# Performance work log

Hardware: AMD Instinct MI355X
Metric: run time of the kernel (lower is better)

Reference implementation:

```python
import jax, jax.numpy as jnp
import numpy as np

B, L, R, K = 4, 512, 512, 16
DN, DE = 128, 64
HOPI, CNNC = 32, 32


def _conv2d(x, w, b, pad):
    # x: (B,C,H,W), w: (O,I,kh,kw)
    y = jax.lax.conv_general_dilated(x, w, (1, 1), [(pad, pad), (pad, pad)],
                                     dimension_numbers=('NCHW', 'OIHW', 'NCHW'))
    return y + b[None, :, None, None]


def setup_inputs() -> dict:
    key = jax.random.key(0)
    ks = jax.random.split(key, 16)
    s = lambda d: 1.0 / np.sqrt(d)
    inp = {
        'ligand_node_features': jax.random.normal(ks[0], (B, L, DN), jnp.float32),
        'ligand_edge_features': jax.random.normal(ks[1], (B, L, K, DE), jnp.float32),
        'receptor_node_features': jax.random.normal(ks[2], (B, R, DN), jnp.float32),
        'receptor_edge_features': jax.random.normal(ks[3], (B, R, K, DE), jnp.float32),
        # GNN params
        'WN': jax.random.uniform(ks[4], (DN, DN), jnp.float32, -s(DN), s(DN)),
        'bN': jax.random.uniform(ks[5], (DN,), jnp.float32, -s(DN), s(DN)),
        'WE': jax.random.uniform(ks[6], (DN, DE), jnp.float32, -s(DE), s(DE)),
        'bE': jax.random.uniform(ks[7], (DN,), jnp.float32, -s(DE), s(DE)),
        # HOPI linear: (out, 2*DN)
        'Wp': jax.random.uniform(ks[8], (HOPI, 2 * DN), jnp.float32, -s(2 * DN), s(2 * DN)),
        'bp': jax.random.uniform(ks[9], (HOPI,), jnp.float32, -s(2 * DN), s(2 * DN)),
        # CNN params
        'Wc1': jax.random.uniform(ks[10], (CNNC, HOPI, 3, 3), jnp.float32, -s(HOPI * 9), s(HOPI * 9)),
        'bc1': jax.random.uniform(ks[11], (CNNC,), jnp.float32, -s(HOPI * 9), s(HOPI * 9)),
        'Wc2': jax.random.uniform(ks[12], (CNNC, CNNC, 3, 3), jnp.float32, -s(CNNC * 9), s(CNNC * 9)),
        'bc2': jax.random.uniform(ks[13], (CNNC,), jnp.float32, -s(CNNC * 9), s(CNNC * 9)),
        'Wc3': jax.random.uniform(ks[14], (1, CNNC, 1, 1), jnp.float32, -s(CNNC), s(CNNC)),
        'bc3': jax.random.uniform(ks[15], (1,), jnp.float32, -s(CNNC), s(CNNC)),
    }
    return inp


def _gnn(node, edge, WN, bN, WE, bE):
    # node: (B,N,DN), edge: (B,N,K,DE) -> (B,N,DN)
    hn = jnp.einsum('bnd,od->bno', node, WN) + bN          # (B,N,DN)
    he = jnp.einsum('bnke,oe->bnko', edge, WE) + bE        # (B,N,K,DN)
    Z = jnp.tanh(hn[:, :, None, :] + he)                   # (B,N,K,DN)
    return node + Z.mean(axis=2)


def reference(ligand_node_features, ligand_edge_features, receptor_node_features,
              receptor_edge_features, WN, bN, WE, bE, Wp, bp,
              Wc1, bc1, Wc2, bc2, Wc3, bc3):
    lig = _gnn(ligand_node_features, ligand_edge_features, WN, bN, WE, bE)      # (B,L,DN)
    rec = _gnn(receptor_node_features, receptor_edge_features, WN, bN, WE, bE)  # (B,R,DN)
    # HOPI: linear(cat(lig_i, rec_j)) = lig@Wl^T + rec@Wr^T + b, broadcast over pairs
    Wl, Wr = Wp[:, :DN], Wp[:, DN:]
    pl = jnp.einsum('bld,od->blo', lig, Wl)                 # (B,L,HOPI)
    pr = jnp.einsum('brd,od->bro', rec, Wr)                 # (B,R,HOPI)
    P = pl[:, :, None, :] + pr[:, None, :, :] + bp          # (B,L,R,HOPI)
    x = jnp.transpose(P, (0, 3, 1, 2))                      # (B,HOPI,L,R)
    x = jax.nn.relu(_conv2d(x, Wc1, bc1, 1))
    x = jax.nn.relu(_conv2d(x, Wc2, bc2, 1))
    x = _conv2d(x, Wc3, bc3, 0)                             # (B,1,L,R)
    return jax.nn.sigmoid(x)[:, 0]                          # (B,L,R)
```

## Files before the change

### kernel.cpp

```cpp
#include <hip/hip_runtime.h>
#include <hip/hip_bf16.h>
#include <math.h>


typedef __attribute__((ext_vector_type(8))) short short8v;
typedef __attribute__((ext_vector_type(4))) float f32x4;

__device__ __forceinline__ unsigned pack_bf16_2(float x, float y) {
    __hip_bfloat16 hx = __float2bfloat16(x);
    __hip_bfloat16 hy = __float2bfloat16(y);
    unsigned short ux = *(unsigned short*)&hx;
    unsigned short uy = *(unsigned short*)&hy;
    return (unsigned)ux | ((unsigned)uy << 16);
}

__global__ __launch_bounds__(256) void prep_weights(
    const float* __restrict__ Wc1, const float* __restrict__ Wc2,
    const float* __restrict__ WN, const float* __restrict__ WE,
    const float* __restrict__ Wp,
    float* __restrict__ WA, float* __restrict__ WB,
    unsigned short* __restrict__ W2F,
    float* __restrict__ WN4, float* __restrict__ WE4,
    float* __restrict__ WpT4)
{
    const int t = blockIdx.x * 256 + threadIdx.x;

    if (t < 9216) {
        const int f    = t >> 9;
        const int lane = (t >> 3) & 63;
        const int j    = t & 7;
        const int tap  = f >> 1;
        const int h    = f & 1;
        const int co   = h * 16 + (lane & 15);
        const int ci   = (lane >> 4) * 8 + j;
        const float w  = Wc2[(co * 32 + ci) * 9 + tap];
        __hip_bfloat16 hb = __float2bfloat16(w);
        W2F[t] = *(unsigned short*)&hb;

        const int tap1 = t >> 10;
        const int ci1  = (t >> 5) & 31;
        const int co1  = t & 31;
        if (tap1 < 3) {
            const int k = tap1;
            const float* w1 = Wc1 + (co1 * 32 + ci1) * 9;
            float w0 = w1[k * 3 + 0], wq = w1[k * 3 + 1], w2 = w1[k * 3 + 2];
            WA[((0 * 3 + k) * 32 + ci1) * 32 + co1] = wq + w2;
            WA[((1 * 3 + k) * 32 + ci1) * 32 + co1] = w0 + wq + w2;
            WA[((2 * 3 + k) * 32 + ci1) * 32 + co1] = w0 + wq;
            float q0 = w1[0 * 3 + k], q1 = w1[1 * 3 + k], q2 = w1[2 * 3 + k];
            WB[((0 * 3 + k) * 32 + ci1) * 32 + co1] = q1 + q2;
            WB[((1 * 3 + k) * 32 + ci1) * 32 + co1] = q0 + q1 + q2;
            WB[((2 * 3 + k) * 32 + ci1) * 32 + co1] = q0 + q1;
        }
    }
    if (t < 16384) {
        const int d4 = t >> 9, o = (t >> 2) & 127, j = t & 3;
        WN4[t] = WN[o * 128 + d4 * 4 + j];
    }
    if (t < 8192) {
        const int e4 = t >> 9, o = (t >> 2) & 127, j = t & 3;
        WE4[t] = WE[o * 64 + e4 * 4 + j];
    }
    if (t < 8192) {
        const int d4 = t >> 8, c = (t >> 2) & 63, j = t & 3;
        const int s = c >> 5, po = c & 31;
        WpT4[t] = Wp[po * 256 + s * 128 + d4 * 4 + j];
    }
}

__global__ __launch_bounds__(128, 4) void gnn_proj_kernel(
    const float* __restrict__ lig_node, const float* __restrict__ lig_edge,
    const float* __restrict__ rec_node, const float* __restrict__ rec_edge,
    const float* __restrict__ WN4, const float* __restrict__ bN,
    const float* __restrict__ WE4, const float* __restrict__ bE,
    const float* __restrict__ WpT4, const float* __restrict__ bp,
    float* __restrict__ pl, float* __restrict__ prb)
{
    const int blk  = blockIdx.x;
    const int side = blk >> 11;
    const int b    = (blk >> 9) & 3;
    const int n    = blk & 511;
    const float* node = (side ? rec_node : lig_node) + (b * 512 + n) * 128;
    const float* edge = (side ? rec_edge : lig_edge) + (b * 512 + n) * 1024;

    __shared__ float s_node[128];
    __shared__ float s_edge[1024];
    __shared__ float s_out[128];

    const int tid = threadIdx.x;
    s_node[tid] = node[tid];
    ((float4*)s_edge)[tid]       = ((const float4*)edge)[tid];
    ((float4*)s_edge)[tid + 128] = ((const float4*)edge)[tid + 128];
    __syncthreads();

    const int o = tid;

    float4 h4 = make_float4(0.f, 0.f, 0.f, 0.f);
    const float4* wn4 = (const float4*)WN4 + o;
    const float4* sn4 = (const float4*)s_node;
    #pragma unroll 1
    for (int d4 = 0; d4 < 32; ++d4) {
        const float4 w = wn4[d4 * 128];
        const float4 x = sn4[d4];
        h4.x = fmaf(w.x, x.x, h4.x);
        h4.y = fmaf(w.y, x.y, h4.y);
        h4.z = fmaf(w.z, x.z, h4.z);
        h4.w = fmaf(w.w, x.w, h4.w);
    }
    const float base = (h4.x + h4.y) + (h4.z + h4.w) + bN[o] + bE[o];

    float acc[16];
    #pragma unroll
    for (int k = 0; k < 16; ++k) acc[k] = 0.f;
    const float4* we4 = (const float4*)WE4 + o;
    const float4* se4 = (const float4*)s_edge;
    #pragma unroll 1
    for (int e4 = 0; e4 < 16; ++e4) {
        const float4 w = we4[e4 * 128];
        #pragma unroll
        for (int k = 0; k < 16; ++k) {
            const float4 s = se4[k * 16 + e4];
            acc[k] = fmaf(w.x, s.x, fmaf(w.y, s.y,
                     fmaf(w.z, s.z, fmaf(w.w, s.w, acc[k]))));
        }
    }

    float ssum = 0.f;
    #pragma unroll
    for (int k = 0; k < 16; ++k) {
        const float ex = __expf(2.f * (base + acc[k]));
        ssum += 1.f - 2.f * __builtin_amdgcn_rcpf(ex + 1.f);
    }
    s_out[o] = s_node[o] + ssum * 0.0625f;
    __syncthreads();

    if (tid < 32) {
        const int c = side * 32 + tid;
        const float4* wp4 = (const float4*)WpT4 + c;
        const float4* so4 = (const float4*)s_out;
        float4 a4 = make_float4(0.f, 0.f, 0.f, 0.f);
        #pragma unroll 1
        for (int d4 = 0; d4 < 32; ++d4) {
            const float4 w = wp4[d4 * 64];
            const float4 x = so4[d4];
            a4.x = fmaf(w.x, x.x, a4.x);
            a4.y = fmaf(w.y, x.y, a4.y);
            a4.z = fmaf(w.z, x.z, a4.z);
            a4.w = fmaf(w.w, x.w, a4.w);
        }
        const float vv = (a4.x + a4.y) + (a4.z + a4.w) + (side ? bp[tid] : 0.f);
        (side ? prb : pl)[(b * 512 + n) * 32 + tid] = vv;
    }
}

__global__ __launch_bounds__(256) void uv_kernel(
    const float* __restrict__ pl, const float* __restrict__ prb,
    const float* __restrict__ WA, const float* __restrict__ WB,
    const float* __restrict__ bc1,
    float* __restrict__ u, float* __restrict__ v)
{
    const int idx = blockIdx.x * 256 + threadIdx.x;
    const int uv = idx >> 16;
    const int b  = (idx >> 14) & 3;
    const int l  = (idx >> 5) & 511;
    const int co = idx & 31;

    const float* p = (uv ? prb : pl) + (b * 512) * 32;
    const float* W = (uv ? WB : WA);
    float acc0 = uv ? 0.f : bc1[co];
    float acc1 = acc0, acc2 = acc0;
    #pragma unroll
    for (int d = 0; d < 3; ++d) {
        const int ln = l + d - 1;
        if (ln < 0 || ln >= 512) continue;
        const float* pv = p + ln * 32;
        const float* w0 = W + ((0 * 3 + d) * 32) * 32 + co;
        const float* w1 = W + ((1 * 3 + d) * 32) * 32 + co;
        const float* w2 = W + ((2 * 3 + d) * 32) * 32 + co;
        #pragma unroll
        for (int ci = 0; ci < 32; ++ci) {
            const float x = pv[ci];
            acc0 = fmaf(w0[ci * 32], x, acc0);
            acc1 = fmaf(w1[ci * 32], x, acc1);
            acc2 = fmaf(w2[ci * 32], x, acc2);
        }
    }
    float* dst = uv ? v : u;
    const int base = (b * 512 + l) * 32 + co;
    dst[0 * 65536 + base] = acc0;
    dst[1 * 65536 + base] = acc1;
    dst[2 * 65536 + base] = acc2;
}

__global__ __launch_bounds__(256) void conv_fused_kernel(
    const float* __restrict__ u, const float* __restrict__ v,
    const unsigned short* __restrict__ W2F,
    const float* __restrict__ bc2,
    const float* __restrict__ Wc3, const float* __restrict__ bc3,
    float* __restrict__ out)
{
    const int tc = blockIdx.x, tr = blockIdx.y, b = blockIdx.z;
    const int l0 = tr * 16, r0 = tc * 16;
    __shared__ unsigned short sY1[324 * 40];
    __shared__ float sU[18 * 36];
    __shared__ float sV[18 * 36];
    const int tid = threadIdx.x;

    for (int t = tid; t < 288; t += 256) {
        const int which = (t >= 144);
        const int s = which ? t - 144 : t;
        const int row = s >> 3, c4 = s & 7;
        const int pos = (which ? r0 : l0) - 1 + row;
        float4 val = make_float4(0.f, 0.f, 0.f, 0.f);
        if (pos >= 0 && pos < 512) {
            const float* src = (which ? v : u) + ((1 * 4 + b) * 512 + pos) * 32;
            val = ((const float4*)src)[c4];
        }
        ((float4*)((which ? sV : sU) + row * 36))[c4] = val;
    }
    __syncthreads();

    for (int p = tid; p < 324; p += 256) {
        const int i = p / 18, j = p - i * 18;
        const int l = l0 + i - 1, r = r0 + j - 1;
        uint4 q0 = make_uint4(0u, 0u, 0u, 0u), q1 = q0, q2 = q0, q3 = q0;
        if ((l >= 0) & (l < 512) & (r >= 0) & (r < 512)) {
            float y[32];
            const bool edge = (r == 0) | (r == 511) | (l == 0) | (l == 511);
            if (!edge) {
                const float4* up = (const float4*)&sU[i * 36];
                const float4* vp = (const float4*)&sV[j * 36];
                #pragma unroll
                for (int c4 = 0; c4 < 8; ++c4) {
                    const float4 a = up[c4], q = vp[c4];
                    y[c4 * 4 + 0] = fmaxf(a.x + q.x, 0.f);
                    y[c4 * 4 + 1] = fmaxf(a.y + q.y, 0.f);
                    y[c4 * 4 + 2] = fmaxf(a.z + q.z, 0.f);
                    y[c4 * 4 + 3] = fmaxf(a.w + q.w, 0.f);
                }
            } else {
                const int cr = (r == 0) ? 0 : (r == 511) ? 2 : 1;
                const int cl = (l == 0) ? 0 : (l == 511) ? 2 : 1;
                const float4* up = (const float4*)&u[((cr * 4 + b) * 512 + l) * 32];
                const float4* vp = (const float4*)&v[((cl * 4 + b) * 512 + r) * 32];
                #pragma unroll
                for (int c4 = 0; c4 < 8; ++c4) {
                    const float4 a = up[c4], q = vp[c4];
                    y[c4 * 4 + 0] = fmaxf(a.x + q.x, 0.f);
                    y[c4 * 4 + 1] = fmaxf(a.y + q.y, 0.f);
                    y[c4 * 4 + 2] = fmaxf(a.z + q.z, 0.f);
                    y[c4 * 4 + 3] = fmaxf(a.w + q.w, 0.f);
                }
            }
            q0 = make_uint4(pack_bf16_2(y[0], y[1]),  pack_bf16_2(y[2], y[3]),
                            pack_bf16_2(y[4], y[5]),  pack_bf16_2(y[6], y[7]));
            q1 = make_uint4(pack_bf16_2(y[8], y[9]),  pack_bf16_2(y[10], y[11]),
                            pack_bf16_2(y[12], y[13]), pack_bf16_2(y[14], y[15]));
            q2 = make_uint4(pack_bf16_2(y[16], y[17]), pack_bf16_2(y[18], y[19]),
                            pack_bf16_2(y[20], y[21]), pack_bf16_2(y[22], y[23]));
            q3 = make_uint4(pack_bf16_2(y[24], y[25]), pack_bf16_2(y[26], y[27]),
                            pack_bf16_2(y[28], y[29]), pack_bf16_2(y[30], y[31]));
        }
        uint4* dst = (uint4*)&sY1[p * 40];
        dst[0] = q0; dst[1] = q1; dst[2] = q2; dst[3] = q3;
    }

    const int lane = tid & 63;
    const int wv   = tid >> 6;
    const int m    = lane & 15;
    const int kc   = lane >> 4;
    short8v bf[18];
    #pragma unroll
    for (int f = 0; f < 18; ++f)
        bf[f] = *(const short8v*)&W2F[(f * 64 + lane) * 8];
    const float bc2_0 = bc2[m],      bc2_1 = bc2[m + 16];
    const float wc3_0 = Wc3[m],      wc3_1 = Wc3[m + 16];
    const float bc3v  = bc3[0];

    __syncthreads();

    #pragma unroll 1
    for (int i = 0; i < 4; ++i) {
        const int ty = wv * 4 + i;
        f32x4 acc0 = {0.f, 0.f, 0.f, 0.f};
        f32x4 acc1 = {0.f, 0.f, 0.f, 0.f};
        #pragma unroll
        for (int dy = 0; dy < 3; ++dy) {
            #pragma unroll
            for (int dx = 0; dx < 3; ++dx) {
                const short8v a = *(const short8v*)
                    &sY1[((ty + dy) * 18 + m + dx) * 40 + kc * 8];
                const int t = dy * 3 + dx;
                acc0 = __builtin_amdgcn_mfma_f32_16x16x32_bf16(a, bf[t * 2 + 0], acc0, 0, 0, 0);
                acc1 = __builtin_amdgcn_mfma_f32_16x16x32_bf16(a, bf[t * 2 + 1], acc1, 0, 0, 0);
            }
        }
        #pragma unroll
        for (int reg = 0; reg < 4; ++reg) {
            float vlt = fmaxf(acc0[reg] + bc2_0, 0.f) * wc3_0
                      + fmaxf(acc1[reg] + bc2_1, 0.f) * wc3_1;
            #pragma unroll
            for (int s = 1; s < 16; s <<= 1)
                vlt += __shfl_xor(vlt, s, 64);
            if (m == reg) {
                const int tx = kc * 4 + reg;
                const float sig = 1.f / (1.f + expf(-(vlt + bc3v)));
                out[(b * 512 + l0 + ty) * 512 + (r0 + tx)] = sig;
            }
        }
    }
}

extern "C" void kernel_launch(void* const* d_in, const int* in_sizes, int n_in,
                              void* d_out, int out_size, void* d_ws, size_t ws_size,
                              hipStream_t stream) {
    const float* lig_node = (const float*)d_in[0];
    const float* lig_edge = (const float*)d_in[1];
    const float* rec_node = (const float*)d_in[2];
    const float* rec_edge = (const float*)d_in[3];
    const float* WN  = (const float*)d_in[4];
    const float* bN  = (const float*)d_in[5];
    const float* WE  = (const float*)d_in[6];
    const float* bE  = (const float*)d_in[7];
    const float* Wp  = (const float*)d_in[8];
    const float* bp  = (const float*)d_in[9];
    const float* Wc1 = (const float*)d_in[10];
    const float* bc1 = (const float*)d_in[11];
    const float* Wc2 = (const float*)d_in[12];
    const float* bc2 = (const float*)d_in[13];
    const float* Wc3 = (const float*)d_in[14];
    const float* bc3 = (const float*)d_in[15];
    float* out = (float*)d_out;

    float* ws  = (float*)d_ws;
    float* pl   = ws;
    float* prb  = ws + 65536;
    float* WA   = ws + 131072;
    float* WB   = ws + 140288;
    unsigned short* W2F = (unsigned short*)(ws + 149504);
    float* u    = ws + 158720;
    float* v    = ws + 355328;
    float* WN4  = ws + 551936;
    float* WE4  = ws + 568320;
    float* WpT4 = ws + 576512;

    hipLaunchKernelGGL(prep_weights, dim3(64), dim3(256), 0, stream,
                       Wc1, Wc2, WN, WE, Wp, WA, WB, W2F, WN4, WE4, WpT4);
    hipLaunchKernelGGL(gnn_proj_kernel, dim3(4096), dim3(128), 0, stream,
                       lig_node, lig_edge, rec_node, rec_edge,
                       WN4, bN, WE4, bE, WpT4, bp, pl, prb);
    hipLaunchKernelGGL(uv_kernel, dim3(512), dim3(256), 0, stream,
                       pl, prb, WA, WB, bc1, u, v);
    hipLaunchKernelGGL(conv_fused_kernel, dim3(32, 32, 4), dim3(256), 0, stream,
                       u, v, W2F, bc2, Wc3, bc3, out);
}
```

Baseline: 187.4 us.

## Process four column tiles per conv block with double-buffered V prefetch

Each conv block now handles four consecutive 16-column tiles instead of one. The sU row data and the B-fragment weight registers are loaded once and reused across all four tiles, while the next tile's V halo rows are prefetched into a second shared buffer during the current tile's build. Blocks that do not touch the image border skip the per-pixel boundary checks. The aim is to amortize per-block setup and weight loads, at the cost of a 4x smaller grid (1024 blocks) and an extra barrier per tile.

```diff
diff --git a/kernel.cpp b/kernel.cpp
--- a/kernel.cpp
+++ b/kernel.cpp
@@ -199,70 +199,25 @@
     const float* __restrict__ Wc3, const float* __restrict__ bc3,
     float* __restrict__ out)
 {
-    const int tc = blockIdx.x, tr = blockIdx.y, b = blockIdx.z;
-    const int l0 = tr * 16, r0 = tc * 16;
+    const int x = blockIdx.x, tr = blockIdx.y, b = blockIdx.z;
+    const int l0 = tr * 16;
     __shared__ unsigned short sY1[324 * 40];
     __shared__ float sU[18 * 36];
-    __shared__ float sV[18 * 36];
+    __shared__ float sV[2][18 * 36];
     const int tid = threadIdx.x;
+    const bool edge_block = (x == 0) | (x == 7) | (tr == 0) | (tr == 31);
 
     for (int t = tid; t < 288; t += 256) {
         const int which = (t >= 144);
         const int s = which ? t - 144 : t;
         const int row = s >> 3, c4 = s & 7;
-        const int pos = (which ? r0 : l0) - 1 + row;
+        const int pos = (which ? x * 64 : l0) - 1 + row;
         float4 val = make_float4(0.f, 0.f, 0.f, 0.f);
         if (pos >= 0 && pos < 512) {
             const float* src = (which ? v : u) + ((1 * 4 + b) * 512 + pos) * 32;
             val = ((const float4*)src)[c4];
         }
-        ((float4*)((which ? sV : sU) + row * 36))[c4] = val;
-    }
-    __syncthreads();
-
-    for (int p = tid; p < 324; p += 256) {
-        const int i = p / 18, j = p - i * 18;
-        const int l = l0 + i - 1, r = r0 + j - 1;
-        uint4 q0 = make_uint4(0u, 0u, 0u, 0u), q1 = q0, q2 = q0, q3 = q0;
-        if ((l >= 0) & (l < 512) & (r >= 0) & (r < 512)) {
-            float y[32];
-            const bool edge = (r == 0) | (r == 511) | (l == 0) | (l == 511);
-            if (!edge) {
-                const float4* up = (const float4*)&sU[i * 36];
-                const float4* vp = (const float4*)&sV[j * 36];
-                #pragma unroll
-                for (int c4 = 0; c4 < 8; ++c4) {
-                    const float4 a = up[c4], q = vp[c4];
-                    y[c4 * 4 + 0] = fmaxf(a.x + q.x, 0.f);
-                    y[c4 * 4 + 1] = fmaxf(a.y + q.y, 0.f);
-                    y[c4 * 4 + 2] = fmaxf(a.z + q.z, 0.f);
-                    y[c4 * 4 + 3] = fmaxf(a.w + q.w, 0.f);
-                }
-            } else {
-                const int cr = (r == 0) ? 0 : (r == 511) ? 2 : 1;
-                const int cl = (l == 0) ? 0 : (l == 511) ? 2 : 1;
-                const float4* up = (const float4*)&u[((cr * 4 + b) * 512 + l) * 32];
-                const float4* vp = (const float4*)&v[((cl * 4 + b) * 512 + r) * 32];
-                #pragma unroll
-                for (int c4 = 0; c4 < 8; ++c4) {
-                    const float4 a = up[c4], q = vp[c4];
-                    y[c4 * 4 + 0] = fmaxf(a.x + q.x, 0.f);
-                    y[c4 * 4 + 1] = fmaxf(a.y + q.y, 0.f);
-                    y[c4 * 4 + 2] = fmaxf(a.z + q.z, 0.f);
-                    y[c4 * 4 + 3] = fmaxf(a.w + q.w, 0.f);
-                }
-            }
-            q0 = make_uint4(pack_bf16_2(y[0], y[1]),  pack_bf16_2(y[2], y[3]),
-                            pack_bf16_2(y[4], y[5]),  pack_bf16_2(y[6], y[7]));
-            q1 = make_uint4(pack_bf16_2(y[8], y[9]),  pack_bf16_2(y[10], y[11]),
-                            pack_bf16_2(y[12], y[13]), pack_bf16_2(y[14], y[15]));
-            q2 = make_uint4(pack_bf16_2(y[16], y[17]), pack_bf16_2(y[18], y[19]),
-                            pack_bf16_2(y[20], y[21]), pack_bf16_2(y[22], y[23]));
-            q3 = make_uint4(pack_bf16_2(y[24], y[25]), pack_bf16_2(y[26], y[27]),
-                            pack_bf16_2(y[28], y[29]), pack_bf16_2(y[30], y[31]));
-        }
-        uint4* dst = (uint4*)&sY1[p * 40];
-        dst[0] = q0; dst[1] = q1; dst[2] = q2; dst[3] = q3;
+        ((float4*)((which ? sV[0] : sU) + row * 36))[c4] = val;
     }
 
     const int lane = tid & 63;
@@ -280,34 +235,127 @@
     __syncthreads();
 
     #pragma unroll 1
-    for (int i = 0; i < 4; ++i) {
-        const int ty = wv * 4 + i;
-        f32x4 acc0 = {0.f, 0.f, 0.f, 0.f};
-        f32x4 acc1 = {0.f, 0.f, 0.f, 0.f};
-        #pragma unroll
-        for (int dy = 0; dy < 3; ++dy) {
+    for (int tt = 0; tt < 4; ++tt) {
+        const int r0 = (x * 4 + tt) * 16;
+        const float* sVc = sV[tt & 1];
+
+        float4 pref = make_float4(0.f, 0.f, 0.f, 0.f);
+        const bool do_pref = (tt < 3) && (tid < 144);
+        int prow = 0, pc4 = 0;
+        if (do_pref) {
+            prow = tid >> 3; pc4 = tid & 7;
+            const int pos = r0 + 15 + prow;
+            if (pos < 512)
+                pref = ((const float4*)&v[((1 * 4 + b) * 512 + pos) * 32])[pc4];
+        }
+
+        if (!edge_block) {
+            for (int p = tid; p < 324; p += 256) {
+                const int i = p / 18, j = p - i * 18;
+                const float4* up = (const float4*)&sU[i * 36];
+                const float4* vp = (const float4*)&sVc[j * 36];
+                float y[32];
+                #pragma unroll
+                for (int c4 = 0; c4 < 8; ++c4) {
+                    const float4 a = up[c4], q = vp[c4];
+                    y[c4 * 4 + 0] = fmaxf(a.x + q.x, 0.f);
+                    y[c4 * 4 + 1] = fmaxf(a.y + q.y, 0.f);
+                    y[c4 * 4 + 2] = fmaxf(a.z + q.z, 0.f);
+                    y[c4 * 4 + 3] = fmaxf(a.w + q.w, 0.f);
+                }
+                uint4* dst = (uint4*)&sY1[p * 40];
+                dst[0] = make_uint4(pack_bf16_2(y[0], y[1]),  pack_bf16_2(y[2], y[3]),
+                                    pack_bf16_2(y[4], y[5]),  pack_bf16_2(y[6], y[7]));
+                dst[1] = make_uint4(pack_bf16_2(y[8], y[9]),  pack_bf16_2(y[10], y[11]),
+                                    pack_bf16_2(y[12], y[13]), pack_bf16_2(y[14], y[15]));
+                dst[2] = make_uint4(pack_bf16_2(y[16], y[17]), pack_bf16_2(y[18], y[19]),
+                                    pack_bf16_2(y[20], y[21]), pack_bf16_2(y[22], y[23]));
+                dst[3] = make_uint4(pack_bf16_2(y[24], y[25]), pack_bf16_2(y[26], y[27]),
+                                    pack_bf16_2(y[28], y[29]), pack_bf16_2(y[30], y[31]));
+            }
+        } else {
+            for (int p = tid; p < 324; p += 256) {
+                const int i = p / 18, j = p - i * 18;
+                const int l = l0 + i - 1, r = r0 + j - 1;
+                uint4 q0 = make_uint4(0u,0u,0u,0u), q1 = q0, q2 = q0, q3 = q0;
+                if ((l >= 0) & (l < 512) & (r >= 0) & (r < 512)) {
+                    float y[32];
+                    const bool edge = (r == 0) | (r == 511) | (l == 0) | (l == 511);
+                    if (!edge) {
+                        const float4* up = (const float4*)&sU[i * 36];
+                        const float4* vp = (const float4*)&sVc[j * 36];
+                        #pragma unroll
+                        for (int c4 = 0; c4 < 8; ++c4) {
+                            const float4 a = up[c4], q = vp[c4];
+                            y[c4 * 4 + 0] = fmaxf(a.x + q.x, 0.f);
+                            y[c4 * 4 + 1] = fmaxf(a.y + q.y, 0.f);
+                            y[c4 * 4 + 2] = fmaxf(a.z + q.z, 0.f);
+                            y[c4 * 4 + 3] = fmaxf(a.w + q.w, 0.f);
+                        }
+                    } else {
+                        const int cr = (r == 0) ? 0 : (r == 511) ? 2 : 1;
+                        const int cl = (l == 0) ? 0 : (l == 511) ? 2 : 1;
+                        const float4* up = (const float4*)&u[((cr * 4 + b) * 512 + l) * 32];
+                        const float4* vp = (const float4*)&v[((cl * 4 + b) * 512 + r) * 32];
+                        #pragma unroll
+                        for (int c4 = 0; c4 < 8; ++c4) {
+                            const float4 a = up[c4], q = vp[c4];
+                            y[c4 * 4 + 0] = fmaxf(a.x + q.x, 0.f);
+                            y[c4 * 4 + 1] = fmaxf(a.y + q.y, 0.f);
+                            y[c4 * 4 + 2] = fmaxf(a.z + q.z, 0.f);
+                            y[c4 * 4 + 3] = fmaxf(a.w + q.w, 0.f);
+                        }
+                    }
+                    q0 = make_uint4(pack_bf16_2(y[0], y[1]),  pack_bf16_2(y[2], y[3]),
+                                    pack_bf16_2(y[4], y[5]),  pack_bf16_2(y[6], y[7]));
+                    q1 = make_uint4(pack_bf16_2(y[8], y[9]),  pack_bf16_2(y[10], y[11]),
+                                    pack_bf16_2(y[12], y[13]), pack_bf16_2(y[14], y[15]));
+                    q2 = make_uint4(pack_bf16_2(y[16], y[17]), pack_bf16_2(y[18], y[19]),
+                                    pack_bf16_2(y[20], y[21]), pack_bf16_2(y[22], y[23]));
+                    q3 = make_uint4(pack_bf16_2(y[24], y[25]), pack_bf16_2(y[26], y[27]),
+                                    pack_bf16_2(y[28], y[29]), pack_bf16_2(y[30], y[31]));
+                }
+                uint4* dst = (uint4*)&sY1[p * 40];
+                dst[0] = q0; dst[1] = q1; dst[2] = q2; dst[3] = q3;
+            }
+        }
+
+        if (do_pref)
+            ((float4*)(sV[(tt + 1) & 1] + prow * 36))[pc4] = pref;
+
+        __syncthreads();
+
+        #pragma unroll 1
+        for (int i = 0; i < 4; ++i) {
+            const int ty = wv * 4 + i;
+            f32x4 acc0 = {0.f, 0.f, 0.f, 0.f};
+            f32x4 acc1 = {0.f, 0.f, 0.f, 0.f};
             #pragma unroll
-            for (int dx = 0; dx < 3; ++dx) {
-                const short8v a = *(const short8v*)
-                    &sY1[((ty + dy) * 18 + m + dx) * 40 + kc * 8];
-                const int t = dy * 3 + dx;
-                acc0 = __builtin_amdgcn_mfma_f32_16x16x32_bf16(a, bf[t * 2 + 0], acc0, 0, 0, 0);
-                acc1 = __builtin_amdgcn_mfma_f32_16x16x32_bf16(a, bf[t * 2 + 1], acc1, 0, 0, 0);
+            for (int dy = 0; dy < 3; ++dy) {
+                #pragma unroll
+                for (int dx = 0; dx < 3; ++dx) {
+                    const short8v a = *(const short8v*)
+                        &sY1[((ty + dy) * 18 + m + dx) * 40 + kc * 8];
+                    const int t = dy * 3 + dx;
+                    acc0 = __builtin_amdgcn_mfma_f32_16x16x32_bf16(a, bf[t * 2 + 0], acc0, 0, 0, 0);
+                    acc1 = __builtin_amdgcn_mfma_f32_16x16x32_bf16(a, bf[t * 2 + 1], acc1, 0, 0, 0);
+                }
             }
-        }
-        #pragma unroll
-        for (int reg = 0; reg < 4; ++reg) {
-            float vlt = fmaxf(acc0[reg] + bc2_0, 0.f) * wc3_0
-                      + fmaxf(acc1[reg] + bc2_1, 0.f) * wc3_1;
             #pragma unroll
-            for (int s = 1; s < 16; s <<= 1)
-                vlt += __shfl_xor(vlt, s, 64);
-            if (m == reg) {
-                const int tx = kc * 4 + reg;
-                const float sig = 1.f / (1.f + expf(-(vlt + bc3v)));
-                out[(b * 512 + l0 + ty) * 512 + (r0 + tx)] = sig;
+            for (int reg = 0; reg < 4; ++reg) {
+                float vlt = fmaxf(acc0[reg] + bc2_0, 0.f) * wc3_0
+                          + fmaxf(acc1[reg] + bc2_1, 0.f) * wc3_1;
+                #pragma unroll
+                for (int s = 1; s < 16; s <<= 1)
+                    vlt += __shfl_xor(vlt, s, 64);
+                if (m == reg) {
+                    const int tx = kc * 4 + reg;
+                    const float sig = 1.f / (1.f + expf(-(vlt + bc3v)));
+                    out[(b * 512 + l0 + ty) * 512 + (r0 + tx)] = sig;
+                }
             }
         }
+        __syncthreads();
     }
 }
 
@@ -351,6 +399,6 @@
                        WN4, bN, WE4, bE, WpT4, bp, pl, prb);
     hipLaunchKernelGGL(uv_kernel, dim3(512), dim3(256), 0, stream,
                        pl, prb, WA, WB, bc1, u, v);
-    hipLaunchKernelGGL(conv_fused_kernel, dim3(32, 32, 4), dim3(256), 0, stream,
+    hipLaunchKernelGGL(conv_fused_kernel, dim3(8, 32, 4), dim3(256), 0, stream,
                        u, v, W2F, bc2, Wc3, bc3, out);
 }
```

After: 201.9 us. 1.08x slower.
